# Kernel tuning notes

Hardware: AMD Instinct MI355X
Metric: run time of the kernel (lower is better)

The kernel has to match this reference:

```python
import jax, jax.numpy as jnp
import numpy as np
from jax import lax

DN = ('NCHW', 'OIHW', 'NCHW')


def setup_inputs() -> dict:
    key = jax.random.key(0)
    ks = jax.random.split(key, 5)
    B, C, H, W = 1, 128, 64, 64
    heads = 4
    return {
        'x_q': jax.random.normal(ks[0], (B, C, H, W), jnp.float32),
        'x_kv': jax.random.normal(ks[1], (B, C, H, W), jnp.float32),
        'w_qkv': jax.random.normal(ks[2], (3 * C, C, 1, 1), jnp.float32) * 0.05,
        'w_dw': jax.random.normal(ks[3], (3 * C, 1, 3, 3), jnp.float32) * 0.2,
        'w_proj': jax.random.normal(ks[4], (C, C, 1, 1), jnp.float32) * 0.05,
        'temperature': jnp.ones((heads, 1, 1), jnp.float32),
    }


def reference(x_q, x_kv, w_qkv, w_dw, w_proj, temperature):
    B, C, H, W = x_q.shape
    heads = temperature.shape[0]
    hd = C // heads
    N = H * W

    # shared qkv 1x1 conv + depthwise 3x3 conv on concatenated [2B,C,H,W]
    x = jnp.concatenate([x_q, x_kv], axis=0)
    qkv = lax.conv_general_dilated(x, w_qkv, (1, 1), 'VALID', dimension_numbers=DN)
    qkv = lax.conv_general_dilated(qkv, w_dw, (1, 1), 'SAME',
                                   feature_group_count=3 * C, dimension_numbers=DN)
    q, k, v = jnp.split(qkv, 3, axis=1)
    q = q[:B]          # query branch from x_q
    k = k[B:]          # key/value branch from x_kv
    v = v[B:]

    def to_heads(t):   # [B,C,H,W] -> [B,h,N,d]
        return t.reshape(B, heads, hd, N).transpose(0, 1, 3, 2)

    attn = jnp.einsum('bhnd,bhmd->bhnm', to_heads(q), to_heads(k)) * temperature
    attn = jax.nn.softmax(attn, axis=-1)
    out = jnp.einsum('bhnm,bhmd->bhnd', attn, to_heads(v))
    out = out.transpose(0, 1, 3, 2).reshape(B, C, H, W)
    return lax.conv_general_dilated(out, w_proj, (1, 1), 'VALID', dimension_numbers=DN)
```

## Files before the change

kernel.cpp:

```cpp
#include <hip/hip_runtime.h>

typedef short bf16x4 __attribute__((ext_vector_type(4)));
typedef short bf16x8 __attribute__((ext_vector_type(8)));
typedef float f32x4 __attribute__((ext_vector_type(4)));
typedef unsigned short u16x4 __attribute__((ext_vector_type(4)));
typedef unsigned short u16x8 __attribute__((ext_vector_type(8)));

__device__ __forceinline__ unsigned short f2bf(float f) {
  union { float f; unsigned u; } v; v.f = f;
  unsigned r = v.u + 0x7FFFu + ((v.u >> 16) & 1u);
  return (unsigned short)(r >> 16);
}
__device__ __forceinline__ unsigned fbits(float f) {
  union { float f; unsigned u; } x; x.f = f; return x.u;
}
__device__ __forceinline__ float bfloat(unsigned u) {
  union { unsigned u; float f; } x; x.u = u; return x.f;
}
__device__ __forceinline__ float fexp2(float x) {
#if __has_builtin(__builtin_amdgcn_exp2f)
  return __builtin_amdgcn_exp2f(x);
#else
  return exp2f(x);
#endif
}
__device__ __forceinline__ f32x4 pv_mfma(bf16x4 a, bf16x4 b, f32x4 c) {
#if __has_builtin(__builtin_amdgcn_mfma_f32_16x16x16bf16_1k)
  return __builtin_amdgcn_mfma_f32_16x16x16bf16_1k(a, b, c, 0, 0, 0);
#else
  bf16x8 az = {a[0], a[1], a[2], a[3], 0, 0, 0, 0};
  bf16x8 bz = {b[0], b[1], b[2], b[3], 0, 0, 0, 0};
  return __builtin_amdgcn_mfma_f32_16x16x32_bf16(az, bz, c, 0, 0, 0);
#endif
}

__global__ __launch_bounds__(256)
void cast_kernel(const float* __restrict__ Xq, const float* __restrict__ Xkv,
                 const float* __restrict__ Wqkv, const float* __restrict__ Wproj,
                 unsigned short* __restrict__ XT, unsigned short* __restrict__ Wq16,
                 unsigned short* __restrict__ Wph, unsigned short* __restrict__ Wpl)
{
  const int b = blockIdx.x, t = threadIdx.x;
  if (b < 256) {
    __shared__ __align__(16) float Tl[64][68];
    const int img = b >> 7, kt = (b >> 6) & 1, nt = b & 63;
    const float* X = img ? Xkv : Xq;
    #pragma unroll
    for (int i = 0; i < 4; ++i) {
      int e = i * 256 + t;
      int r = e >> 4, c4 = (e & 15) * 4;
      *(f32x4*)&Tl[r][c4] = *(const f32x4*)&X[(kt * 64 + r) * 4096 + nt * 64 + c4];
    }
    __syncthreads();
    unsigned short* out = XT + img * (4096 * 128);
    #pragma unroll
    for (int i = 0; i < 2; ++i) {
      int u = i * 256 + t;
      int n = u >> 3, kg = u & 7;
      u16x8 tv;
      #pragma unroll
      for (int j = 0; j < 8; ++j) tv[j] = f2bf(Tl[kg * 8 + j][n]);
      *(u16x8*)&out[(nt * 64 + n) * 128 + kt * 64 + kg * 8] = tv;
    }
  } else {
    const int wb = b - 256;
    if (wb < 3) {
      #pragma unroll 4
      for (int i = 0; i < 64; ++i) {
        int idx = wb * 16384 + i * 256 + t;
        Wq16[idx] = f2bf(Wqkv[idx]);
      }
    } else {
      #pragma unroll 4
      for (int i = 0; i < 64; ++i) {
        int idx = i * 256 + t;
        float v = Wproj[idx];
        unsigned short h = f2bf(v);
        float hf = bfloat((unsigned)h << 16);
        Wph[idx] = h;
        Wpl[idx] = f2bf(v - hf);
      }
    }
  }
}

__global__ __launch_bounds__(256)
void gemm_qkv_kernel(const unsigned short* __restrict__ XT,
                     const unsigned short* __restrict__ Wq16,
                     unsigned short* __restrict__ Y16)
{
  const int t = threadIdx.x;
  const int w = t >> 6, c = t & 15, g = (t & 63) >> 4;
  const int n0 = blockIdx.x * 32;
  const int ob = blockIdx.y;
  const int o_base = ob * 64 + w * 16;
  const unsigned short* B = XT + (ob >= 2 ? 4096 * 128 : 0);
  f32x4 acc0 = {0.f, 0.f, 0.f, 0.f}, acc1 = {0.f, 0.f, 0.f, 0.f};
  #pragma unroll
  for (int ks = 0; ks < 4; ++ks) {
    bf16x8 a = *(const bf16x8*)&Wq16[(o_base + c) * 128 + ks * 32 + g * 8];
    bf16x8 b0 = *(const bf16x8*)&B[(n0 + c) * 128 + ks * 32 + g * 8];
    bf16x8 b1 = *(const bf16x8*)&B[(n0 + 16 + c) * 128 + ks * 32 + g * 8];
    acc0 = __builtin_amdgcn_mfma_f32_16x16x32_bf16(a, b0, acc0, 0, 0, 0);
    acc1 = __builtin_amdgcn_mfma_f32_16x16x32_bf16(a, b1, acc1, 0, 0, 0);
  }
  #pragma unroll
  for (int i = 0; i < 4; ++i) {
    Y16[(o_base + 4 * g + i) * 4096 + n0 + c] = f2bf(acc0[i]);
    Y16[(o_base + 4 * g + i) * 4096 + n0 + 16 + c] = f2bf(acc1[i]);
  }
}

__global__ __launch_bounds__(256)
void gemm_proj_kernel(const unsigned short* __restrict__ Oth,
                      const unsigned short* __restrict__ Otl,
                      const unsigned short* __restrict__ Wph,
                      const unsigned short* __restrict__ Wpl, float* __restrict__ Y)
{
  const int t = threadIdx.x;
  const int w = t >> 6, c = t & 15, g = (t & 63) >> 4;
  const int n0 = blockIdx.x * 32;
  const int o_base = blockIdx.y * 64 + w * 16;
  f32x4 acc0 = {0.f, 0.f, 0.f, 0.f}, acc1 = {0.f, 0.f, 0.f, 0.f};
  #pragma unroll
  for (int ks = 0; ks < 4; ++ks) {
    const int ko = ks * 32 + g * 8;
    bf16x8 ah = *(const bf16x8*)&Wph[(o_base + c) * 128 + ko];
    bf16x8 al = *(const bf16x8*)&Wpl[(o_base + c) * 128 + ko];
    bf16x8 bh0 = *(const bf16x8*)&Oth[(n0 + c) * 128 + ko];
    bf16x8 bl0 = *(const bf16x8*)&Otl[(n0 + c) * 128 + ko];
    bf16x8 bh1 = *(const bf16x8*)&Oth[(n0 + 16 + c) * 128 + ko];
    bf16x8 bl1 = *(const bf16x8*)&Otl[(n0 + 16 + c) * 128 + ko];
    acc0 = __builtin_amdgcn_mfma_f32_16x16x32_bf16(al, bh0, acc0, 0, 0, 0);
    acc0 = __builtin_amdgcn_mfma_f32_16x16x32_bf16(ah, bl0, acc0, 0, 0, 0);
    acc0 = __builtin_amdgcn_mfma_f32_16x16x32_bf16(ah, bh0, acc0, 0, 0, 0);
    acc1 = __builtin_amdgcn_mfma_f32_16x16x32_bf16(al, bh1, acc1, 0, 0, 0);
    acc1 = __builtin_amdgcn_mfma_f32_16x16x32_bf16(ah, bl1, acc1, 0, 0, 0);
    acc1 = __builtin_amdgcn_mfma_f32_16x16x32_bf16(ah, bh1, acc1, 0, 0, 0);
  }
  #pragma unroll
  for (int i = 0; i < 4; ++i) {
    Y[(o_base + 4 * g + i) * 4096 + n0 + c] = acc0[i];
    Y[(o_base + 4 * g + i) * 4096 + n0 + 16 + c] = acc1[i];
  }
}

__global__ __launch_bounds__(256)
void dwconv_kernel(const unsigned short* __restrict__ T16, const float* __restrict__ Wd,
                   const float* __restrict__ temp, unsigned short* __restrict__ Qb)
{
  __shared__ __align__(16) float P[4096];
  const int jc = blockIdx.x;
  const int t = threadIdx.x;
  const unsigned short* in = T16 + jc * 4096;
  #pragma unroll
  for (int i = 0; i < 2; ++i) {
    u16x8 v = *(const u16x8*)&in[(i * 256 + t) * 8];
    #pragma unroll
    for (int j = 0; j < 8; ++j)
      P[(i * 256 + t) * 8 + j] = bfloat((unsigned)v[j] << 16);
  }
  float w[9];
  #pragma unroll
  for (int k = 0; k < 9; ++k) w[k] = Wd[jc * 9 + k];
  const float scale = (jc < 128) ? temp[jc >> 5] * 1.4426950408889634f : 1.0f;
  __syncthreads();
  unsigned short* out = Qb + jc * 4096;
  #pragma unroll 4
  for (int i = 0; i < 16; ++i) {
    int idx = i * 256 + t;
    int y = idx >> 6, x = idx & 63;
    float acc = 0.f;
    #pragma unroll
    for (int dy = -1; dy <= 1; ++dy) {
      int yy = y + dy;
      if (yy < 0 || yy > 63) continue;
      #pragma unroll
      for (int dx = -1; dx <= 1; ++dx) {
        int xx = x + dx;
        if (xx < 0 || xx > 63) continue;
        acc += w[(dy + 1) * 3 + (dx + 1)] * P[yy * 64 + xx];
      }
    }
    out[idx] = f2bf(acc * scale);
  }
}

#define KOFF (128 * 4096)
#define VOFF (256 * 4096)
#define KSTR 40
#define VSTR 132

__global__ __launch_bounds__(1024, 4)
void attn_kernel(const unsigned short* __restrict__ Qb,
                 unsigned short* __restrict__ Oth, unsigned short* __restrict__ Otl)
{
  __shared__ __align__(16) char lds[74752];
  unsigned short* Kg = (unsigned short*)lds;
  unsigned short* Vg = (unsigned short*)(lds + 40960);
  const int t = threadIdx.x;
  const int g4 = t >> 8;
  const int ts = t & 255;
  const int qw = (t >> 6) & 3;
  const int l = t & 63;
  const int c = l & 15, g = l >> 4;
  const int h = blockIdx.y;
  const int nq = blockIdx.x * 64;

  unsigned short* Kgg = Kg + g4 * (128 * KSTR);
  unsigned short* Vgg = Vg + g4 * (32 * VSTR);

  bf16x8 qf[4];
  #pragma unroll
  for (int s = 0; s < 4; ++s)
    #pragma unroll
    for (int e = 0; e < 8; ++e)
      qf[s][e] = (short)Qb[(h * 32 + g * 8 + e) * 4096 + nq + s * 16 + c];

  f32x4 oh[4][2];
  #pragma unroll
  for (int s = 0; s < 4; ++s) {
    oh[s][0] = (f32x4){0.f, 0.f, 0.f, 0.f};
    oh[s][1] = (f32x4){0.f, 0.f, 0.f, 0.f};
  }
  float lsum[4] = {0.f, 0.f, 0.f, 0.f};

  const int kdp = ts >> 4;
  const int kj  = ts & 15;
  const int vdd = ts >> 4;
  const int vj  = ts & 15;

  u16x4 kr0[2], kr1[2];
  u16x8 vr[2];
  {
    const int m0 = g4 * 128;
    #pragma unroll
    for (int it = 0; it < 2; ++it) {
      int m = kj * 4 + it * 64;
      kr0[it] = *(const u16x4*)&Qb[KOFF + (h * 32 + 2 * kdp) * 4096 + m0 + m];
      kr1[it] = *(const u16x4*)&Qb[KOFF + (h * 32 + 2 * kdp + 1) * 4096 + m0 + m];
      vr[it] = *(const u16x8*)&Qb[VOFF + (h * 32 + vdd + 16 * it) * 4096 + m0 + vj * 8];
    }
  }

  for (int tt = 0; tt < 8; ++tt) {
    __syncthreads();
    #pragma unroll
    for (int it = 0; it < 2; ++it) {
      int m = kj * 4 + it * 64;
      #pragma unroll
      for (int i = 0; i < 4; ++i)
        *(unsigned*)&Kgg[(m + i) * KSTR + 2 * kdp] =
            (unsigned)kr0[it][i] | ((unsigned)kr1[it][i] << 16);
      int d = vdd + 16 * it;
      *(u16x4*)&Vgg[d * VSTR + vj * 8] =
          __builtin_shufflevector(vr[it], vr[it], 0, 1, 2, 3);
      *(u16x4*)&Vgg[d * VSTR + vj * 8 + 4] =
          __builtin_shufflevector(vr[it], vr[it], 4, 5, 6, 7);
    }
    __syncthreads();
    if (tt < 7) {
      const int m0n = ((tt + 1) * 4 + g4) * 128;
      #pragma unroll
      for (int it = 0; it < 2; ++it) {
        int m = kj * 4 + it * 64;
        kr0[it] = *(const u16x4*)&Qb[KOFF + (h * 32 + 2 * kdp) * 4096 + m0n + m];
        kr1[it] = *(const u16x4*)&Qb[KOFF + (h * 32 + 2 * kdp + 1) * 4096 + m0n + m];
        vr[it] = *(const u16x8*)&Qb[VOFF + (h * 32 + vdd + 16 * it) * 4096 + m0n + vj * 8];
      }
    }
    #pragma unroll
    for (int jj = 0; jj < 2; ++jj) {
      const int j = qw * 2 + jj;
      bf16x8 kf = *(const bf16x8*)&Kgg[(j * 16 + c) * KSTR + g * 8];
      bf16x4 vf0 = *(const bf16x4*)&Vgg[c * VSTR + j * 16 + g * 4];
      bf16x4 vf1 = *(const bf16x4*)&Vgg[(16 + c) * VSTR + j * 16 + g * 4];
      #pragma unroll
      for (int s = 0; s < 4; ++s) {
        f32x4 z = {0.f, 0.f, 0.f, 0.f};
        f32x4 sv = __builtin_amdgcn_mfma_f32_16x16x32_bf16(kf, qf[s], z, 0, 0, 0);
        unsigned u0 = fbits(fexp2(sv[0]));
        unsigned u1 = fbits(fexp2(sv[1]));
        unsigned u2 = fbits(fexp2(sv[2]));
        unsigned u3 = fbits(fexp2(sv[3]));
        unsigned t0 = u0 & 0xFFFF0000u, t1 = u1 & 0xFFFF0000u;
        unsigned t2 = u2 & 0xFFFF0000u, t3 = u3 & 0xFFFF0000u;
        lsum[s] += (bfloat(t0) + bfloat(t1)) + (bfloat(t2) + bfloat(t3));
        unsigned pk0 = (u0 >> 16) | t1;
        unsigned pk1 = (u2 >> 16) | t3;
        union { unsigned u[2]; bf16x4 v; } pu;
        pu.u[0] = pk0; pu.u[1] = pk1;
        oh[s][0] = pv_mfma(vf0, pu.v, oh[s][0]);
        oh[s][1] = pv_mfma(vf1, pu.v, oh[s][1]);
      }
    }
  }

  #pragma unroll
  for (int s = 0; s < 4; ++s) {
    lsum[s] += __shfl_xor(lsum[s], 16, 64);
    lsum[s] += __shfl_xor(lsum[s], 32, 64);
  }

  __syncthreads();
  float* OG  = (float*)lds;
  float* lfq = (float*)(lds + 34048);
  float* lf  = (float*)(lds + 36864);
  if (l < 16) {
    #pragma unroll
    for (int s = 0; s < 4; ++s)
      lf[(g4 * 4 + qw) * 64 + s * 16 + c] = lsum[s];
  }
  for (int r = 0; r < 4; ++r) {
    if (qw == r) {
      #pragma unroll
      for (int s = 0; s < 4; ++s)
        #pragma unroll
        for (int i = 0; i < 4; ++i) {
          int d0 = 4 * g + i;
          float* p0 = &OG[g4 * 2112 + d0 * 66 + s * 16 + c];
          float* p1 = &OG[g4 * 2112 + (16 + d0) * 66 + s * 16 + c];
          if (r == 0) { *p0 = oh[s][0][i];  *p1 = oh[s][1][i]; }
          else        { *p0 += oh[s][0][i]; *p1 += oh[s][1][i]; }
        }
    }
    __syncthreads();
  }
  if (t < 64) {
    float a = 0.f;
    #pragma unroll
    for (int ww = 0; ww < 16; ++ww) a += lf[ww * 64 + t];
    lfq[t] = a;
  }
  __syncthreads();

  #pragma unroll
  for (int e = t; e < 2048; e += 1024) {
    int d = e & 31, q = e >> 5;
    float s4 = OG[0 * 2112 + d * 66 + q] + OG[1 * 2112 + d * 66 + q] +
               OG[2 * 2112 + d * 66 + q] + OG[3 * 2112 + d * 66 + q];
    float val = s4 / lfq[q];
    unsigned short hi = f2bf(val);
    float hf = bfloat((unsigned)hi << 16);
    int idx = (blockIdx.x * 64 + q) * 128 + h * 32 + d;
    Oth[idx] = hi;
    Otl[idx] = f2bf(val - hf);
  }
}

extern "C" void kernel_launch(void* const* d_in, const int* in_sizes, int n_in,
                              void* d_out, int out_size, void* d_ws, size_t ws_size,
                              hipStream_t stream) {
  const float* xq    = (const float*)d_in[0];
  const float* xkv   = (const float*)d_in[1];
  const float* wqkv  = (const float*)d_in[2];
  const float* wdw   = (const float*)d_in[3];
  const float* wproj = (const float*)d_in[4];
  const float* temp  = (const float*)d_in[5];
  float* out = (float*)d_out;

  char* ws = (char*)d_ws;
  unsigned short* t16  = (unsigned short*)ws;
  unsigned short* qb   = (unsigned short*)(ws + 3145728);
  unsigned short* xt   = (unsigned short*)(ws + 6291456);
  unsigned short* wq16 = (unsigned short*)(ws + 8388608);
  unsigned short* wph  = (unsigned short*)(ws + 8486912);
  unsigned short* wpl  = (unsigned short*)(ws + 8519680);
  unsigned short* oth  = (unsigned short*)(ws + 8552448);
  unsigned short* otl  = (unsigned short*)(ws + 9601024);

  cast_kernel<<<dim3(260), 256, 0, stream>>>(xq, xkv, wqkv, wproj, xt, wq16, wph, wpl);
  gemm_qkv_kernel<<<dim3(128, 6), 256, 0, stream>>>(xt, wq16, t16);
  dwconv_kernel<<<dim3(384), 256, 0, stream>>>(t16, wdw, temp, qb);
  attn_kernel<<<dim3(64, 4), 1024, 0, stream>>>(qb, oth, otl);
  gemm_proj_kernel<<<dim3(128, 2), 256, 0, stream>>>(oth, otl, wph, wpl, out);
}
```

Baseline: 62.34 us.

## Load K/V fragments directly from global memory per wave, dropping LDS staging

The attention loop no longer stages K and V tiles through shared memory with double-buffered register prefetch and two barriers per tile. Each of the 16 waves instead owns a contiguous 256-key slice and reads its K and V MFMA fragments straight from global memory. The goal is to remove the barriers and the LDS write/read traffic, and to shrink shared memory to only what the epilogue needs. The cost is that K is now fetched as strided 2-byte gathers that depend on cache hits, and latency is no longer hidden by explicit prefetch. The bf16 packing of the probabilities also moves to a single byte-permute instruction.

New measurement: 57.39 us. 1.09x faster.

```diff
diff --git a/kernel.cpp b/kernel.cpp
--- a/kernel.cpp
+++ b/kernel.cpp
@@ -188,27 +188,20 @@
 
 #define KOFF (128 * 4096)
 #define VOFF (256 * 4096)
-#define KSTR 40
-#define VSTR 132
 
 __global__ __launch_bounds__(1024, 4)
 void attn_kernel(const unsigned short* __restrict__ Qb,
                  unsigned short* __restrict__ Oth, unsigned short* __restrict__ Otl)
 {
-  __shared__ __align__(16) char lds[74752];
-  unsigned short* Kg = (unsigned short*)lds;
-  unsigned short* Vg = (unsigned short*)(lds + 40960);
+  __shared__ __align__(16) char lds[40960];
   const int t = threadIdx.x;
-  const int g4 = t >> 8;
-  const int ts = t & 255;
-  const int qw = (t >> 6) & 3;
+  const int wv = t >> 6;
+  const int g4 = wv >> 2, qw = wv & 3;
   const int l = t & 63;
   const int c = l & 15, g = l >> 4;
   const int h = blockIdx.y;
   const int nq = blockIdx.x * 64;
-
-  unsigned short* Kgg = Kg + g4 * (128 * KSTR);
-  unsigned short* Vgg = Vg + g4 * (32 * VSTR);
+  const int m0w = wv * 256;
 
   bf16x8 qf[4];
   #pragma unroll
@@ -225,74 +218,34 @@
   }
   float lsum[4] = {0.f, 0.f, 0.f, 0.f};
 
-  const int kdp = ts >> 4;
-  const int kj  = ts & 15;
-  const int vdd = ts >> 4;
-  const int vj  = ts & 15;
-
-  u16x4 kr0[2], kr1[2];
-  u16x8 vr[2];
-  {
-    const int m0 = g4 * 128;
-    #pragma unroll
-    for (int it = 0; it < 2; ++it) {
-      int m = kj * 4 + it * 64;
-      kr0[it] = *(const u16x4*)&Qb[KOFF + (h * 32 + 2 * kdp) * 4096 + m0 + m];
-      kr1[it] = *(const u16x4*)&Qb[KOFF + (h * 32 + 2 * kdp + 1) * 4096 + m0 + m];
-      vr[it] = *(const u16x8*)&Qb[VOFF + (h * 32 + vdd + 16 * it) * 4096 + m0 + vj * 8];
-    }
-  }
-
-  for (int tt = 0; tt < 8; ++tt) {
-    __syncthreads();
-    #pragma unroll
-    for (int it = 0; it < 2; ++it) {
-      int m = kj * 4 + it * 64;
-      #pragma unroll
-      for (int i = 0; i < 4; ++i)
-        *(unsigned*)&Kgg[(m + i) * KSTR + 2 * kdp] =
-            (unsigned)kr0[it][i] | ((unsigned)kr1[it][i] << 16);
-      int d = vdd + 16 * it;
-      *(u16x4*)&Vgg[d * VSTR + vj * 8] =
-          __builtin_shufflevector(vr[it], vr[it], 0, 1, 2, 3);
-      *(u16x4*)&Vgg[d * VSTR + vj * 8 + 4] =
-          __builtin_shufflevector(vr[it], vr[it], 4, 5, 6, 7);
-    }
-    __syncthreads();
-    if (tt < 7) {
-      const int m0n = ((tt + 1) * 4 + g4) * 128;
-      #pragma unroll
-      for (int it = 0; it < 2; ++it) {
-        int m = kj * 4 + it * 64;
-        kr0[it] = *(const u16x4*)&Qb[KOFF + (h * 32 + 2 * kdp) * 4096 + m0n + m];
-        kr1[it] = *(const u16x4*)&Qb[KOFF + (h * 32 + 2 * kdp + 1) * 4096 + m0n + m];
-        vr[it] = *(const u16x8*)&Qb[VOFF + (h * 32 + vdd + 16 * it) * 4096 + m0n + vj * 8];
-      }
-    }
-    #pragma unroll
-    for (int jj = 0; jj < 2; ++jj) {
-      const int j = qw * 2 + jj;
-      bf16x8 kf = *(const bf16x8*)&Kgg[(j * 16 + c) * KSTR + g * 8];
-      bf16x4 vf0 = *(const bf16x4*)&Vgg[c * VSTR + j * 16 + g * 4];
-      bf16x4 vf1 = *(const bf16x4*)&Vgg[(16 + c) * VSTR + j * 16 + g * 4];
-      #pragma unroll
-      for (int s = 0; s < 4; ++s) {
-        f32x4 z = {0.f, 0.f, 0.f, 0.f};
-        f32x4 sv = __builtin_amdgcn_mfma_f32_16x16x32_bf16(kf, qf[s], z, 0, 0, 0);
-        unsigned u0 = fbits(fexp2(sv[0]));
-        unsigned u1 = fbits(fexp2(sv[1]));
-        unsigned u2 = fbits(fexp2(sv[2]));
-        unsigned u3 = fbits(fexp2(sv[3]));
-        unsigned t0 = u0 & 0xFFFF0000u, t1 = u1 & 0xFFFF0000u;
-        unsigned t2 = u2 & 0xFFFF0000u, t3 = u3 & 0xFFFF0000u;
-        lsum[s] += (bfloat(t0) + bfloat(t1)) + (bfloat(t2) + bfloat(t3));
-        unsigned pk0 = (u0 >> 16) | t1;
-        unsigned pk1 = (u2 >> 16) | t3;
-        union { unsigned u[2]; bf16x4 v; } pu;
-        pu.u[0] = pk0; pu.u[1] = pk1;
-        oh[s][0] = pv_mfma(vf0, pu.v, oh[s][0]);
-        oh[s][1] = pv_mfma(vf1, pu.v, oh[s][1]);
-      }
+  const unsigned short* Kb = Qb + KOFF + (h * 32 + g * 8) * 4096 + m0w + c;
+  const unsigned short* Vb0 = Qb + VOFF + (h * 32 + c) * 4096 + m0w + g * 4;
+  const unsigned short* Vb1 = Vb0 + 16 * 4096;
+
+  #pragma unroll 4
+  for (int j = 0; j < 16; ++j) {
+    bf16x8 kf;
+    #pragma unroll
+    for (int e = 0; e < 8; ++e)
+      kf[e] = (short)Kb[e * 4096 + j * 16];
+    bf16x4 vf0 = *(const bf16x4*)&Vb0[j * 16];
+    bf16x4 vf1 = *(const bf16x4*)&Vb1[j * 16];
+    #pragma unroll
+    for (int s = 0; s < 4; ++s) {
+      f32x4 z = {0.f, 0.f, 0.f, 0.f};
+      f32x4 sv = __builtin_amdgcn_mfma_f32_16x16x32_bf16(kf, qf[s], z, 0, 0, 0);
+      unsigned u0 = fbits(fexp2(sv[0]));
+      unsigned u1 = fbits(fexp2(sv[1]));
+      unsigned u2 = fbits(fexp2(sv[2]));
+      unsigned u3 = fbits(fexp2(sv[3]));
+      unsigned t0 = u0 & 0xFFFF0000u, t1 = u1 & 0xFFFF0000u;
+      unsigned t2 = u2 & 0xFFFF0000u, t3 = u3 & 0xFFFF0000u;
+      lsum[s] += (bfloat(t0) + bfloat(t1)) + (bfloat(t2) + bfloat(t3));
+      union { unsigned u[2]; bf16x4 v; } pu;
+      pu.u[0] = __builtin_amdgcn_perm(u1, u0, 0x07060302);
+      pu.u[1] = __builtin_amdgcn_perm(u3, u2, 0x07060302);
+      oh[s][0] = pv_mfma(vf0, pu.v, oh[s][0]);
+      oh[s][1] = pv_mfma(vf1, pu.v, oh[s][1]);
     }
   }
 
```
